# Kernel tuning notes

Measured on AMD Instinct MI355X. Metric: run time of the kernel, lower is better.

The kernel has to match this reference:

```python
import jax, jax.numpy as jnp
import numpy as np

FEATURE_SIZE = 40960
FIRST_HIDDEN = 512
HALF = FIRST_HIDDEN // 2  # 256, per-perspective width
SECOND_HIDDEN = 32
BATCH = 4096


def setup_inputs() -> dict:
    key = jax.random.key(0)
    ks = jax.random.split(key, 10)
    inp = {
        "white_features": jax.random.uniform(ks[0], (BATCH, FEATURE_SIZE), dtype=jnp.float32),
        "black_features": jax.random.uniform(ks[1], (BATCH, FEATURE_SIZE), dtype=jnp.float32),
        # input_layer1 and input_layer2 share weight_float/bias_float -> single param
        "w_in": jax.random.normal(ks[2], (HALF, FEATURE_SIZE), dtype=jnp.float32) * 0.1,
        "b_in": jnp.zeros((HALF,), dtype=jnp.float32),
        "w_h1": jax.random.normal(ks[3], (SECOND_HIDDEN, FIRST_HIDDEN), dtype=jnp.float32) * 0.1,
        "b_h1": jnp.zeros((SECOND_HIDDEN,), dtype=jnp.float32),
        "w_h2": jax.random.normal(ks[4], (SECOND_HIDDEN, SECOND_HIDDEN), dtype=jnp.float32) * 0.1,
        "b_h2": jnp.zeros((SECOND_HIDDEN,), dtype=jnp.float32),
        "w_out": jax.random.normal(ks[5], (1, SECOND_HIDDEN), dtype=jnp.float32) * 0.1,
        "b_out": jnp.zeros((1,), dtype=jnp.float32),
    }
    return inp


def _clipped_relu(x):
    return jnp.clip(x, 0.0, 1.0)


def reference(white_features, black_features, w_in, b_in, w_h1, b_h1, w_h2, b_h2, w_out, b_out):
    # Perspective feature transform (shared weights), training-mode float path
    out1 = white_features @ w_in.T + b_in  # [B, 256]
    out2 = black_features @ w_in.T + b_in  # [B, 256]
    x = _clipped_relu(jnp.concatenate([out1, out2], axis=1))  # [B, 512]
    x = _clipped_relu(x @ w_h1.T + b_h1)  # [B, 32]
    x = _clipped_relu(x @ w_h2.T + b_h2)  # [B, 32]
    return x @ w_out.T + b_out  # [B, 1]
```

## Files before the change

### kernel.cpp

```cpp
#include <hip/hip_runtime.h>
#include <hip/hip_fp16.h>


#define FEAT 40960
#define PSTRIDE (8192ull * 256ull)
#define KSPLIT 8
#define KCHUNK (FEAT / KSPLIT)
#define NSTEP 160
#define WTILE_BYTES 16384
#define WWS_BYTES (1280ull * WTILE_BYTES)

using floatx4 = __attribute__((ext_vector_type(4))) float;
using half8   = __attribute__((ext_vector_type(8))) _Float16;

__global__ __launch_bounds__(256) void nnue_wprep(
    const float* __restrict__ w_in, _Float16* __restrict__ Wws)
{
    const int bid = blockIdx.x;
    const int T   = (bid & 7) * NSTEP + (bid >> 3);
    char* base = (char*)Wws + (size_t)T * WTILE_BYTES;
    const int tid = threadIdx.x;
    const int kg0 = T * 32;
#pragma unroll
    for (int i = 0; i < 4; ++i) {
        const int G = tid + i * 256;
        const int r = G >> 2, g = G & 3;
        const float* src = w_in + (size_t)r * FEAT + kg0 + g * 8;
        floatx4 v0 = *reinterpret_cast<const floatx4*>(src);
        floatx4 v1 = *reinterpret_cast<const floatx4*>(src + 4);
        half8 h;
#pragma unroll
        for (int j = 0; j < 4; ++j) { h[j] = (_Float16)v0[j]; h[4 + j] = (_Float16)v1[j]; }
        *reinterpret_cast<half8*>(base + r * 64 + ((g ^ ((r >> 1) & 3)) << 4)) = h;
    }
}

template <typename PT>
__global__ __launch_bounds__(512, 4) void nnue_gemm_v10(
    const float* __restrict__ white, const float* __restrict__ black,
    const _Float16* __restrict__ Wws, PT* __restrict__ P)
{
    __shared__ __align__(16) _Float16 Ws[4][256 * 32];

    const int tid  = threadIdx.x;
    const int lane = tid & 63;
    const int wave = tid >> 6;

    const int ks = blockIdx.x & 7;
    const int mb = blockIdx.x >> 3;

    const float* Abase = (mb < 32)
        ? (white + (size_t)mb * 128 * FEAT)
        : (black + (size_t)(mb - 32) * 128 * FEAT);
    const int k0 = ks * KCHUNK;

    const int frow = lane & 15;
    const int fhi  = lane >> 4;

    const float* Aptr = Abase + (size_t)(wave * 16 + frow) * FEAT + fhi * 8 + k0;

    const int kb = (fhi * 16) ^ (((frow >> 1) & 3) << 4);

    const char* wsrc0 = (const char*)Wws + (size_t)(ks * NSTEP) * WTILE_BYTES
                        + wave * 2048 + lane * 16;

    floatx4 acc[16];
    const floatx4 zero = {0.f, 0.f, 0.f, 0.f};
#pragma unroll
    for (int n = 0; n < 16; ++n) acc[n] = zero;

    floatx4 cA0, cA1, cA2, cA3, nA0, nA1, nA2, nA3;

    auto issueW = [&](int t, int wb) {
        const char* g = wsrc0 + (size_t)t * WTILE_BYTES;
        char* l = (char*)&Ws[wb][0] + wave * 2048;
        __builtin_amdgcn_global_load_lds(
            (const __attribute__((address_space(1))) unsigned int*)g,
            (__attribute__((address_space(3))) unsigned int*)l, 16, 0, 0);
        __builtin_amdgcn_global_load_lds(
            (const __attribute__((address_space(1))) unsigned int*)(g + 1024),
            (__attribute__((address_space(3))) unsigned int*)(l + 1024), 16, 0, 0);
    };

    auto cvt = [&](const floatx4& a0, const floatx4& a1) {
        half8 h;
#pragma unroll
        for (int j = 0; j < 4; ++j) { h[j] = (_Float16)a0[j]; h[4 + j] = (_Float16)a1[j]; }
        return h;
    };

    auto mfmaStep = [&](int wb, half8 af) {
        const char* wbase = (const char*)&Ws[wb][0];
#pragma unroll
        for (int n = 0; n < 16; ++n) {
            half8 bf = *reinterpret_cast<const half8*>(
                wbase + (n * 16 + frow) * 64 + kb);
            acc[n] = __builtin_amdgcn_mfma_f32_16x16x32_f16(af, bf, acc[n], 0, 0, 0);
        }
    };

    auto groupf = [&](int g,
                      floatx4& c0, floatx4& c1, floatx4& c2, floatx4& c3,
                      floatx4& n0, floatx4& n1, floatx4& n2, floatx4& n3,
                      int rb0, int rb1, int wb0, int wb1) {
        const int t0 = 2 * g;
        issueW(t0 + 2, wb0);
        issueW(t0 + 3, wb1);
        __builtin_amdgcn_sched_barrier(0);
        n0 = *reinterpret_cast<const floatx4*>(Aptr + (size_t)(t0 + 2) * 32);
        n1 = *reinterpret_cast<const floatx4*>(Aptr + (size_t)(t0 + 2) * 32 + 4);
        n2 = *reinterpret_cast<const floatx4*>(Aptr + (size_t)(t0 + 3) * 32);
        n3 = *reinterpret_cast<const floatx4*>(Aptr + (size_t)(t0 + 3) * 32 + 4);
        mfmaStep(rb0, cvt(c0, c1));
        mfmaStep(rb1, cvt(c2, c3));
        asm volatile("s_waitcnt vmcnt(4) lgkmcnt(0)" ::: "memory");
        __builtin_amdgcn_s_barrier();
        __builtin_amdgcn_sched_barrier(0);
    };

    issueW(0, 0);
    issueW(1, 1);
    __builtin_amdgcn_sched_barrier(0);
    cA0 = *reinterpret_cast<const floatx4*>(Aptr);
    cA1 = *reinterpret_cast<const floatx4*>(Aptr + 4);
    cA2 = *reinterpret_cast<const floatx4*>(Aptr + 32);
    cA3 = *reinterpret_cast<const floatx4*>(Aptr + 32 + 4);
    asm volatile("s_waitcnt vmcnt(4)" ::: "memory");
    __builtin_amdgcn_s_barrier();
    __builtin_amdgcn_sched_barrier(0);

    for (int p = 0; p < 39; ++p) {
        groupf(2 * p,     cA0, cA1, cA2, cA3, nA0, nA1, nA2, nA3, 0, 1, 2, 3);
        groupf(2 * p + 1, nA0, nA1, nA2, nA3, cA0, cA1, cA2, cA3, 2, 3, 0, 1);
    }
    groupf(78, cA0, cA1, cA2, cA3, nA0, nA1, nA2, nA3, 0, 1, 2, 3);
    mfmaStep(2, cvt(nA0, nA1));
    mfmaStep(3, cvt(nA2, nA3));

    PT* Pb = P + (size_t)ks * PSTRIDE + (size_t)mb * 128 * 256;
#pragma unroll
    for (int n = 0; n < 16; ++n)
#pragma unroll
        for (int r = 0; r < 4; ++r) {
            const int row = wave * 16 + fhi * 4 + r;
            const int col = n * 16 + frow;
            Pb[(size_t)row * 256 + col] = (PT)acc[n][r];
        }
}

template <typename PT>
__global__ __launch_bounds__(256) void nnue_tail(
    const PT* __restrict__ P,
    const float* __restrict__ b_in,
    const float* __restrict__ w_h1, const float* __restrict__ b_h1,
    const float* __restrict__ w_h2, const float* __restrict__ b_h2,
    const float* __restrict__ w_out, const float* __restrict__ b_out,
    float* __restrict__ out)
{
    __shared__ float xs[32][512];
    __shared__ float w1[32][513];
    __shared__ float w2[32][33];
    __shared__ float h1[32][33];
    __shared__ float h2[32][33];
    __shared__ float wo[32];

    const int tid = threadIdx.x;
    const int b0  = blockIdx.x * 32;

    for (int i = tid; i < 32 * 512; i += 256) w1[i >> 9][i & 511] = w_h1[i];
    for (int i = tid; i < 32 * 32; i += 256)  w2[i >> 5][i & 31]  = w_h2[i];
    if (tid < 32) wo[tid] = w_out[tid];

    for (int i = tid; i < 32 * 512; i += 256) {
        const int r = i >> 9, c = i & 511;
        const int persp = c >> 8, n = c & 255;
        const size_t prow = (size_t)(b0 + r) + (persp ? 4096u : 0u);
        float v = 0.f;
#pragma unroll
        for (int s = 0; s < KSPLIT; ++s)
            v += (float)P[(size_t)s * PSTRIDE + prow * 256 + n];
        v += b_in[n];
        xs[r][c] = fminf(fmaxf(v, 0.f), 1.f);
    }
    __syncthreads();

    for (int p = tid; p < 32 * 32; p += 256) {
        const int o = p & 31, r = p >> 5;
        float a = b_h1[o];
        for (int j = 0; j < 512; ++j) a += xs[r][j] * w1[o][j];
        h1[r][o] = fminf(fmaxf(a, 0.f), 1.f);
    }
    __syncthreads();

    for (int p = tid; p < 32 * 32; p += 256) {
        const int o = p & 31, r = p >> 5;
        float a = b_h2[o];
        for (int j = 0; j < 32; ++j) a += h1[r][j] * w2[o][j];
        h2[r][o] = fminf(fmaxf(a, 0.f), 1.f);
    }
    __syncthreads();

    if (tid < 32) {
        float a = b_out[0];
        for (int j = 0; j < 32; ++j) a += h2[tid][j] * wo[j];
        out[b0 + tid] = a;
    }
}

__global__ __launch_bounds__(256) void nnue_naive(
    const float* __restrict__ white, const float* __restrict__ black,
    const float* __restrict__ w_in, const float* __restrict__ b_in,
    const float* __restrict__ w_h1, const float* __restrict__ b_h1,
    const float* __restrict__ w_h2, const float* __restrict__ b_h2,
    const float* __restrict__ w_out, const float* __restrict__ b_out,
    float* __restrict__ out)
{
    __shared__ float feat[4096];
    __shared__ float xs[512];
    __shared__ float h1s[32];
    __shared__ float h2s[32];
    const int b = blockIdx.x, tid = threadIdx.x;
    float acc0 = 0.f, acc1 = 0.f;
    for (int c = 0; c < FEAT; c += 2048) {
        for (int i = tid; i < 2048; i += 256) {
            feat[i]        = white[(size_t)b * FEAT + c + i];
            feat[2048 + i] = black[(size_t)b * FEAT + c + i];
        }
        __syncthreads();
        const float* wr = w_in + (size_t)tid * FEAT + c;
        for (int k = 0; k < 2048; ++k) {
            const float w = wr[k];
            acc0 += feat[k] * w;
            acc1 += feat[2048 + k] * w;
        }
        __syncthreads();
    }
    xs[tid]       = fminf(fmaxf(acc0 + b_in[tid], 0.f), 1.f);
    xs[256 + tid] = fminf(fmaxf(acc1 + b_in[tid], 0.f), 1.f);
    __syncthreads();
    if (tid < 32) {
        float a = b_h1[tid];
        for (int j = 0; j < 512; ++j) a += xs[j] * w_h1[tid * 512 + j];
        h1s[tid] = fminf(fmaxf(a, 0.f), 1.f);
    }
    __syncthreads();
    if (tid < 32) {
        float a = b_h2[tid];
        for (int j = 0; j < 32; ++j) a += h1s[j] * w_h2[tid * 32 + j];
        h2s[tid] = fminf(fmaxf(a, 0.f), 1.f);
    }
    __syncthreads();
    if (tid == 0) {
        float a = b_out[0];
        for (int j = 0; j < 32; ++j) a += h2s[j] * w_out[j];
        out[b] = a;
    }
}

extern "C" void kernel_launch(void* const* d_in, const int* in_sizes, int n_in,
                              void* d_out, int out_size, void* d_ws, size_t ws_size,
                              hipStream_t stream)
{
    const float* white = (const float*)d_in[0];
    const float* black = (const float*)d_in[1];
    const float* w_in  = (const float*)d_in[2];
    const float* b_in  = (const float*)d_in[3];
    const float* w_h1  = (const float*)d_in[4];
    const float* b_h1  = (const float*)d_in[5];
    const float* w_h2  = (const float*)d_in[6];
    const float* b_h2  = (const float*)d_in[7];
    const float* w_out = (const float*)d_in[8];
    const float* b_out = (const float*)d_in[9];
    float* out = (float*)d_out;

    const size_t pF32 = KSPLIT * PSTRIDE * sizeof(float);
    const size_t pF16 = KSPLIT * PSTRIDE * sizeof(_Float16);

    if (ws_size >= pF32 + WWS_BYTES) {
        float* P = (float*)d_ws;
        _Float16* Wws = (_Float16*)((char*)d_ws + pF32);
        nnue_wprep<<<dim3(1280), 256, 0, stream>>>(w_in, Wws);
        nnue_gemm_v10<float><<<dim3(512), 512, 0, stream>>>(white, black, Wws, P);
        nnue_tail<float><<<dim3(128), 256, 0, stream>>>(P, b_in, w_h1, b_h1,
                                                        w_h2, b_h2, w_out, b_out, out);
    } else if (ws_size >= pF16 + WWS_BYTES) {
        _Float16* P = (_Float16*)d_ws;
        _Float16* Wws = (_Float16*)((char*)d_ws + pF16);
        nnue_wprep<<<dim3(1280), 256, 0, stream>>>(w_in, Wws);
        nnue_gemm_v10<_Float16><<<dim3(512), 512, 0, stream>>>(white, black, Wws, P);
        nnue_tail<_Float16><<<dim3(128), 256, 0, stream>>>(P, b_in, w_h1, b_h1,
                                                           w_h2, b_h2, w_out, b_out, out);
    } else {
        nnue_naive<<<4096, 256, 0, stream>>>(white, black, w_in, b_in, w_h1, b_h1,
                                             w_h2, b_h2, w_out, b_out, out);
    }
}
```

Baseline: 390.4 us.

## Rewrite GEMM to stream weights directly into registers with 32x32 MFMA

The main GEMM no longer stages weight tiles in LDS behind block barriers. Each wave now owns a 32-row strip, loads pre-swizzled fp16 weight fragments straight from global memory into registers with double buffering, and uses 32x32x16 MFMA. Each strip starts at a staggered K offset so that different waves read different weight regions. The grid drops to 256 blocks at 2 waves-per-SIMD occupancy, which removes LDS and sync cost but makes every wave reload the full weight slice from L2.

```diff
diff --git a/kernel.cpp b/kernel.cpp
--- a/kernel.cpp
+++ b/kernel.cpp
@@ -6,145 +6,112 @@
 #define PSTRIDE (8192ull * 256ull)
 #define KSPLIT 8
 #define KCHUNK (FEAT / KSPLIT)
-#define NSTEP 160
-#define WTILE_BYTES 16384
-#define WWS_BYTES (1280ull * WTILE_BYTES)
-
-using floatx4 = __attribute__((ext_vector_type(4))) float;
-using half8   = __attribute__((ext_vector_type(8))) _Float16;
-
-__global__ __launch_bounds__(256) void nnue_wprep(
-    const float* __restrict__ w_in, _Float16* __restrict__ Wws)
-{
-    const int bid = blockIdx.x;
-    const int T   = (bid & 7) * NSTEP + (bid >> 3);
-    char* base = (char*)Wws + (size_t)T * WTILE_BYTES;
-    const int tid = threadIdx.x;
-    const int kg0 = T * 32;
-#pragma unroll
-    for (int i = 0; i < 4; ++i) {
-        const int G = tid + i * 256;
-        const int r = G >> 2, g = G & 3;
-        const float* src = w_in + (size_t)r * FEAT + kg0 + g * 8;
+#define NSTEP16 320
+#define WWS_BYTES (20480ull * 1024ull)
+
+using floatx4  = __attribute__((ext_vector_type(4))) float;
+using floatx16 = __attribute__((ext_vector_type(16))) float;
+using half8    = __attribute__((ext_vector_type(8))) _Float16;
+
+__global__ __launch_bounds__(256) void nnue_wprep32(
+    const float* __restrict__ w_in, _Float16* __restrict__ W2)
+{
+    const int cg = blockIdx.x & 7;
+    const int kw = (blockIdx.x >> 3) * 256;
+    const int c  = cg * 32 + (threadIdx.x >> 3);
+    const int j0 = threadIdx.x & 7;
+#pragma unroll
+    for (int p = 0; p < 4; ++p) {
+        const int k = kw + (j0 + 8 * p) * 8;
+        const float* src = w_in + (size_t)c * FEAT + k;
         floatx4 v0 = *reinterpret_cast<const floatx4*>(src);
         floatx4 v1 = *reinterpret_cast<const floatx4*>(src + 4);
         half8 h;
 #pragma unroll
         for (int j = 0; j < 4; ++j) { h[j] = (_Float16)v0[j]; h[4 + j] = (_Float16)v1[j]; }
-        *reinterpret_cast<half8*>(base + r * 64 + ((g ^ ((r >> 1) & 3)) << 4)) = h;
+        const int ks = k / KCHUNK;
+        const int t  = (k % KCHUNK) >> 4;
+        const int kh = (k >> 3) & 1;
+        const int lw = (kh << 5) | (c & 31);
+        const size_t C = (size_t)(ks * NSTEP16 + t) * 8 + cg;
+        *reinterpret_cast<half8*>((char*)W2 + C * 1024 + lw * 16) = h;
     }
 }
 
 template <typename PT>
-__global__ __launch_bounds__(512, 4) void nnue_gemm_v10(
+__global__ __launch_bounds__(512, 2) void nnue_gemm_v14(
     const float* __restrict__ white, const float* __restrict__ black,
-    const _Float16* __restrict__ Wws, PT* __restrict__ P)
-{
-    __shared__ __align__(16) _Float16 Ws[4][256 * 32];
-
-    const int tid  = threadIdx.x;
-    const int lane = tid & 63;
-    const int wave = tid >> 6;
-
-    const int ks = blockIdx.x & 7;
-    const int mb = blockIdx.x >> 3;
-
-    const float* Abase = (mb < 32)
-        ? (white + (size_t)mb * 128 * FEAT)
-        : (black + (size_t)(mb - 32) * 128 * FEAT);
-    const int k0 = ks * KCHUNK;
-
-    const int frow = lane & 15;
-    const int fhi  = lane >> 4;
-
-    const float* Aptr = Abase + (size_t)(wave * 16 + frow) * FEAT + fhi * 8 + k0;
-
-    const int kb = (fhi * 16) ^ (((frow >> 1) & 3) << 4);
-
-    const char* wsrc0 = (const char*)Wws + (size_t)(ks * NSTEP) * WTILE_BYTES
-                        + wave * 2048 + lane * 16;
-
-    floatx4 acc[16];
-    const floatx4 zero = {0.f, 0.f, 0.f, 0.f};
-#pragma unroll
-    for (int n = 0; n < 16; ++n) acc[n] = zero;
-
-    floatx4 cA0, cA1, cA2, cA3, nA0, nA1, nA2, nA3;
-
-    auto issueW = [&](int t, int wb) {
-        const char* g = wsrc0 + (size_t)t * WTILE_BYTES;
-        char* l = (char*)&Ws[wb][0] + wave * 2048;
-        __builtin_amdgcn_global_load_lds(
-            (const __attribute__((address_space(1))) unsigned int*)g,
-            (__attribute__((address_space(3))) unsigned int*)l, 16, 0, 0);
-        __builtin_amdgcn_global_load_lds(
-            (const __attribute__((address_space(1))) unsigned int*)(g + 1024),
-            (__attribute__((address_space(3))) unsigned int*)(l + 1024), 16, 0, 0);
+    const _Float16* __restrict__ W2, PT* __restrict__ P)
+{
+    const int lane = threadIdx.x & 63;
+    const int wave = threadIdx.x >> 6;
+    const int ks    = blockIdx.x & 7;
+    const int strip = (blockIdx.x >> 3) * 8 + wave;
+
+    const float* Abase = (strip < 128)
+        ? (white + (size_t)strip * 32 * FEAT)
+        : (black + (size_t)(strip - 128) * 32 * FEAT);
+
+    const int row   = lane & 31;
+    const int khalf = lane >> 5;
+    const float* Aptr = Abase + (size_t)row * FEAT + ks * KCHUNK + khalf * 8;
+    const char*  Wbase = (const char*)W2 + (size_t)(ks * NSTEP16) * 8192 + lane * 16;
+
+    floatx16 acc[8];
+#pragma unroll
+    for (int cg = 0; cg < 8; ++cg)
+#pragma unroll
+        for (int r = 0; r < 16; ++r) acc[cg][r] = 0.f;
+
+    const int t0 = (strip * 37) % NSTEP16;
+    auto wrap = [](int x) { return (x >= NSTEP16) ? x - NSTEP16 : x; };
+
+    floatx4 aX0, aX1, aY0, aY1;
+    half8   wX[8], wY[8];
+
+    auto issueA = [&](int t, floatx4& a0, floatx4& a1) {
+        a0 = *reinterpret_cast<const floatx4*>(Aptr + (size_t)t * 16);
+        a1 = *reinterpret_cast<const floatx4*>(Aptr + (size_t)t * 16 + 4);
     };
-
-    auto cvt = [&](const floatx4& a0, const floatx4& a1) {
-        half8 h;
-#pragma unroll
-        for (int j = 0; j < 4; ++j) { h[j] = (_Float16)a0[j]; h[4 + j] = (_Float16)a1[j]; }
-        return h;
+    auto issueW = [&](int t, half8 (&w)[8]) {
+        const char* b = Wbase + (size_t)t * 8192;
+#pragma unroll
+        for (int cg = 0; cg < 8; ++cg)
+            w[cg] = *reinterpret_cast<const half8*>(b + cg * 1024);
     };
-
-    auto mfmaStep = [&](int wb, half8 af) {
-        const char* wbase = (const char*)&Ws[wb][0];
-#pragma unroll
-        for (int n = 0; n < 16; ++n) {
-            half8 bf = *reinterpret_cast<const half8*>(
-                wbase + (n * 16 + frow) * 64 + kb);
-            acc[n] = __builtin_amdgcn_mfma_f32_16x16x32_f16(af, bf, acc[n], 0, 0, 0);
-        }
+    auto consume = [&](floatx4& a0, floatx4& a1, half8 (&w)[8]) {
+        half8 af;
+#pragma unroll
+        for (int j = 0; j < 4; ++j) { af[j] = (_Float16)a0[j]; af[4 + j] = (_Float16)a1[j]; }
+#pragma unroll
+        for (int cg = 0; cg < 8; ++cg)
+            acc[cg] = __builtin_amdgcn_mfma_f32_32x32x16_f16(af, w[cg], acc[cg], 0, 0, 0);
     };
 
-    auto groupf = [&](int g,
-                      floatx4& c0, floatx4& c1, floatx4& c2, floatx4& c3,
-                      floatx4& n0, floatx4& n1, floatx4& n2, floatx4& n3,
-                      int rb0, int rb1, int wb0, int wb1) {
-        const int t0 = 2 * g;
-        issueW(t0 + 2, wb0);
-        issueW(t0 + 3, wb1);
+    issueA(t0, aX0, aX1);
+    issueW(t0, wX);
+    for (int i = 0; i < NSTEP16; i += 2) {
+        const int t1 = wrap(t0 + i + 1);
+        issueA(t1, aY0, aY1);
+        issueW(t1, wY);
         __builtin_amdgcn_sched_barrier(0);
-        n0 = *reinterpret_cast<const floatx4*>(Aptr + (size_t)(t0 + 2) * 32);
-        n1 = *reinterpret_cast<const floatx4*>(Aptr + (size_t)(t0 + 2) * 32 + 4);
-        n2 = *reinterpret_cast<const floatx4*>(Aptr + (size_t)(t0 + 3) * 32);
-        n3 = *reinterpret_cast<const floatx4*>(Aptr + (size_t)(t0 + 3) * 32 + 4);
-        mfmaStep(rb0, cvt(c0, c1));
-        mfmaStep(rb1, cvt(c2, c3));
-        asm volatile("s_waitcnt vmcnt(4) lgkmcnt(0)" ::: "memory");
-        __builtin_amdgcn_s_barrier();
+        consume(aX0, aX1, wX);
+        if (i + 2 < NSTEP16) {
+            const int t2 = wrap(t0 + i + 2);
+            issueA(t2, aX0, aX1);
+            issueW(t2, wX);
+        }
         __builtin_amdgcn_sched_barrier(0);
-    };
-
-    issueW(0, 0);
-    issueW(1, 1);
-    __builtin_amdgcn_sched_barrier(0);
-    cA0 = *reinterpret_cast<const floatx4*>(Aptr);
-    cA1 = *reinterpret_cast<const floatx4*>(Aptr + 4);
-    cA2 = *reinterpret_cast<const floatx4*>(Aptr + 32);
-    cA3 = *reinterpret_cast<const floatx4*>(Aptr + 32 + 4);
-    asm volatile("s_waitcnt vmcnt(4)" ::: "memory");
-    __builtin_amdgcn_s_barrier();
-    __builtin_amdgcn_sched_barrier(0);
-
-    for (int p = 0; p < 39; ++p) {
-        groupf(2 * p,     cA0, cA1, cA2, cA3, nA0, nA1, nA2, nA3, 0, 1, 2, 3);
-        groupf(2 * p + 1, nA0, nA1, nA2, nA3, cA0, cA1, cA2, cA3, 2, 3, 0, 1);
-    }
-    groupf(78, cA0, cA1, cA2, cA3, nA0, nA1, nA2, nA3, 0, 1, 2, 3);
-    mfmaStep(2, cvt(nA0, nA1));
-    mfmaStep(3, cvt(nA2, nA3));
-
-    PT* Pb = P + (size_t)ks * PSTRIDE + (size_t)mb * 128 * 256;
-#pragma unroll
-    for (int n = 0; n < 16; ++n)
-#pragma unroll
-        for (int r = 0; r < 4; ++r) {
-            const int row = wave * 16 + fhi * 4 + r;
-            const int col = n * 16 + frow;
-            Pb[(size_t)row * 256 + col] = (PT)acc[n][r];
+        consume(aY0, aY1, wY);
+    }
+
+    PT* Pb = P + (size_t)ks * PSTRIDE + (size_t)strip * 32 * 256;
+#pragma unroll
+    for (int cg = 0; cg < 8; ++cg)
+#pragma unroll
+        for (int r = 0; r < 16; ++r) {
+            const int rit = (r & 3) + 8 * (r >> 2) + 4 * khalf;
+            Pb[(size_t)rit * 256 + cg * 32 + (lane & 31)] = (PT)acc[cg][r];
         }
 }
 
@@ -278,16 +245,16 @@
 
     if (ws_size >= pF32 + WWS_BYTES) {
         float* P = (float*)d_ws;
-        _Float16* Wws = (_Float16*)((char*)d_ws + pF32);
-        nnue_wprep<<<dim3(1280), 256, 0, stream>>>(w_in, Wws);
-        nnue_gemm_v10<float><<<dim3(512), 512, 0, stream>>>(white, black, Wws, P);
+        _Float16* W2 = (_Float16*)((char*)d_ws + pF32);
+        nnue_wprep32<<<dim3(1280), 256, 0, stream>>>(w_in, W2);
+        nnue_gemm_v14<float><<<dim3(256), 512, 0, stream>>>(white, black, W2, P);
         nnue_tail<float><<<dim3(128), 256, 0, stream>>>(P, b_in, w_h1, b_h1,
                                                         w_h2, b_h2, w_out, b_out, out);
     } else if (ws_size >= pF16 + WWS_BYTES) {
         _Float16* P = (_Float16*)d_ws;
-        _Float16* Wws = (_Float16*)((char*)d_ws + pF16);
-        nnue_wprep<<<dim3(1280), 256, 0, stream>>>(w_in, Wws);
-        nnue_gemm_v10<_Float16><<<dim3(512), 512, 0, stream>>>(white, black, Wws, P);
+        _Float16* W2 = (_Float16*)((char*)d_ws + pF16);
+        nnue_wprep32<<<dim3(1280), 256, 0, stream>>>(w_in, W2);
+        nnue_gemm_v14<_Float16><<<dim3(256), 512, 0, stream>>>(white, black, W2, P);
         nnue_tail<_Float16><<<dim3(128), 256, 0, stream>>>(P, b_in, w_h1, b_h1,
                                                            w_h2, b_h2, w_out, b_out, out);
     } else {
```

After: 629.9 us. +61.3%, slower.
